# Kernel optimization log

Measured on AMD Instinct MI355X. Metric: run time of the kernel, lower is better.

The kernel has to match this reference:

```python
import jax, jax.numpy as jnp
import numpy as np

N_NODES = 100000
N_EDGES = 1600000
IN_CH = 48
OUT_CH = 48
BN_EPS = 1e-5


def setup_inputs() -> dict:
    key = jax.random.key(0)
    k1, k2, k3, k4 = jax.random.split(key, 4)
    x = jax.random.normal(k1, (N_NODES, IN_CH), dtype=jnp.float32)
    edge_index = jax.random.randint(k2, (2, N_EDGES), 0, N_NODES, dtype=jnp.int32)
    # GCNConv linear weight (glorot) and bias
    W = jax.random.normal(k3, (IN_CH, OUT_CH), dtype=jnp.float32) * (1.0 / np.sqrt(IN_CH))
    b = jnp.zeros((OUT_CH,), dtype=jnp.float32)
    # BatchNorm affine params
    gamma = jnp.ones((OUT_CH,), dtype=jnp.float32)
    beta = jnp.zeros((OUT_CH,), dtype=jnp.float32)
    return {"x": x, "edge_index": edge_index, "W": W, "b": b, "gamma": gamma, "beta": beta}


def reference(x, edge_index, W, b, gamma, beta):
    N = x.shape[0]
    # --- GCNConv: add self loops ---
    loops = jnp.arange(N, dtype=edge_index.dtype)
    src = jnp.concatenate([edge_index[0], loops])
    dst = jnp.concatenate([edge_index[1], loops])
    # symmetric normalization: deg counted at destination (incl. self loops)
    deg = jax.ops.segment_sum(jnp.ones_like(dst, dtype=x.dtype), dst, num_segments=N)
    dinv = jax.lax.rsqrt(deg)  # deg >= 1 due to self loops
    norm = dinv[src] * dinv[dst]  # [E+N]
    # linear transform first (small GEMM), then gather-scale-scatter
    h = x @ W  # [N, OUT_CH]
    msg = h[src] * norm[:, None]  # [E+N, OUT_CH]
    agg = jax.ops.segment_sum(msg, dst, num_segments=N) + b  # [N, OUT_CH]
    # --- BatchNorm1d (training mode: batch statistics, biased variance) ---
    mean = jnp.mean(agg, axis=0)
    var = jnp.mean(jnp.square(agg - mean), axis=0)
    y = (agg - mean) * jax.lax.rsqrt(var + BN_EPS) * gamma + beta
    # --- ReLU ---
    return jax.nn.relu(y)
```

## Files before the change

kernel.cpp:

```cpp
#include <hip/hip_runtime.h>
#include <hip/hip_bf16.h>

#define IN_CH 48
#define OUT_CH 48
#define BN_EPS 1e-5f
#define CHUNK 4096
#define EPT   16
#define NPB   256

__device__ __forceinline__ float bf2f(ushort u) {
    union { unsigned int i; float f; } v;
    v.i = ((unsigned int)u) << 16;
    return v.f;
}
__device__ __forceinline__ ushort f2bf(float f) {
    __hip_bfloat16 h = __float2bfloat16(f);
    return *(ushort*)&h;
}

__global__ __launch_bounds__(256) void k_binhist(const int* __restrict__ dst,
                                                 int* __restrict__ bhist, int E) {
    __shared__ int h[512];
    int t = threadIdx.x;
    h[t] = 0; h[t + 256] = 0;
    __syncthreads();
    for (int e = blockIdx.x * 256 + t; e < E; e += gridDim.x * 256)
        atomicAdd(&h[dst[e] >> 8], 1);
    __syncthreads();
    if (h[t]) atomicAdd(&bhist[t], h[t]);
    if (h[t + 256]) atomicAdd(&bhist[t + 256], h[t + 256]);
}

__global__ __launch_bounds__(256) void k_scanb(const int* __restrict__ bhist,
                                               int* __restrict__ bstart,
                                               int* __restrict__ bcur, int nb) {
    __shared__ int sc[256];
    int t = threadIdx.x;
    int i0 = 2 * t, i1 = 2 * t + 1;
    int a0 = bhist[i0];
    int a1 = bhist[i1];
    int ps = a0 + a1;
    sc[t] = ps;
    __syncthreads();
    for (int off = 1; off < 256; off <<= 1) {
        int v = (t >= off) ? sc[t - off] : 0;
        __syncthreads();
        sc[t] += v;
        __syncthreads();
    }
    int excl = sc[t] - ps;
    bstart[i0] = excl;
    bstart[i1] = excl + a0;
    if (i0 < nb) bcur[i0] = excl;
    if (i1 < nb) bcur[i1] = excl + a0;
    if (t == 255) bstart[512] = sc[255];
}

__global__ __launch_bounds__(256) void k_bin(const int* __restrict__ src,
                                             const int* __restrict__ dst,
                                             int* __restrict__ bcur,
                                             unsigned int* __restrict__ binned,
                                             int E) {
    __shared__ int hist[512];
    __shared__ int hbase[513];
    __shared__ int sc[256];
    __shared__ int gb[512];
    __shared__ unsigned int stage[CHUNK];
    __shared__ short stagebk[CHUNK];
    int t = threadIdx.x;
    int e0 = blockIdx.x * CHUNK;
    int n = min(CHUNK, E - e0);

    hist[t] = 0; hist[t + 256] = 0;
    __syncthreads();

    unsigned int w[EPT];
    short bb[EPT];
#pragma unroll
    for (int k = 0; k < EPT; ++k) {
        int i = t + k * 256;
        if (i < n) {
            int e = e0 + i;
            int s = src[e], d = dst[e];
            int b = d >> 8;
            w[k] = (unsigned int)s | ((unsigned int)(d & 255) << 17);
            bb[k] = (short)b;
            atomicAdd(&hist[b], 1);
        } else bb[k] = -1;
    }
    __syncthreads();
    int a0 = hist[2 * t], a1 = hist[2 * t + 1];
    int ps = a0 + a1;
    sc[t] = ps;
    __syncthreads();
    for (int off = 1; off < 256; off <<= 1) {
        int v = (t >= off) ? sc[t - off] : 0;
        __syncthreads();
        sc[t] += v;
        __syncthreads();
    }
    int excl = sc[t] - ps;
    hbase[2 * t] = excl;
    hbase[2 * t + 1] = excl + a0;
    if (t == 255) hbase[512] = sc[255];
    __syncthreads();
    hist[2 * t] = excl;
    hist[2 * t + 1] = excl + a0;
    __syncthreads();
#pragma unroll
    for (int k = 0; k < EPT; ++k) {
        if (bb[k] >= 0) {
            int pos = atomicAdd(&hist[bb[k]], 1);
            stage[pos] = w[k];
            stagebk[pos] = bb[k];
        }
    }
    __syncthreads();
    for (int b = t; b < 512; b += 256) {
        int cnt = hbase[b + 1] - hbase[b];
        if (cnt > 0) gb[b] = atomicAdd(&bcur[b], cnt) - hbase[b];
    }
    __syncthreads();
    for (int j = t; j < n; j += 256) {
        int bk = stagebk[j];
        binned[gb[bk] + j] = stage[j];
    }
}

__global__ __launch_bounds__(512) void k_fine(const unsigned int* __restrict__ binned,
                                              const int* __restrict__ bstart,
                                              int* __restrict__ counts,
                                              int* __restrict__ rowstart,
                                              int* __restrict__ sorted_src, int N) {
    __shared__ int cnt[256];
    __shared__ int sc[256];
    __shared__ int cur[256];
    int b = blockIdx.x, t = threadIdx.x;
    int node0 = b << 8;
    int nn = min(NPB, N - node0);
    if (t < 256) cnt[t] = 0;
    __syncthreads();
    int e0 = bstart[b], e1 = bstart[b + 1];
    for (int e = e0 + t; e < e1; e += 512)
        atomicAdd(&cnt[binned[e] >> 17], 1);
    __syncthreads();
    if (t < 256) sc[t] = cnt[t];
    __syncthreads();
    for (int off = 1; off < 256; off <<= 1) {
        int v = 0;
        if (t < 256 && t >= off) v = sc[t - off];
        __syncthreads();
        if (t < 256) sc[t] += v;
        __syncthreads();
    }
    if (t < 256) {
        int excl = sc[t] - cnt[t];
        cur[t] = e0 + excl;
        if (t < nn) {
            counts[node0 + t] = cnt[t];
            rowstart[node0 + t] = e0 + excl;
        }
    }
    __syncthreads();
    for (int e = e0 + t; e < e1; e += 512) {
        unsigned int w = binned[e];
        int dl = (int)(w >> 17);
        int pos = atomicAdd(&cur[dl], 1);
        sorted_src[pos] = (int)(w & 0x1ffff);
    }
}

__global__ __launch_bounds__(256) void k_gemm(const float* __restrict__ x,
                                              const float* __restrict__ W,
                                              const int* __restrict__ counts,
                                              ushort* __restrict__ g, int N) {
    __shared__ float Wl[IN_CH * OUT_CH];
    for (int idx = threadIdx.x; idx < IN_CH * OUT_CH / 4; idx += blockDim.x)
        ((float4*)Wl)[idx] = ((const float4*)W)[idx];
    __syncthreads();

    int i = blockIdx.x * blockDim.x + threadIdx.x;
    if (i >= N) return;

    float xr[IN_CH];
    const float4* xp = (const float4*)(x + (size_t)i * IN_CH);
#pragma unroll
    for (int k = 0; k < IN_CH / 4; ++k) {
        float4 v = xp[k];
        xr[4 * k] = v.x; xr[4 * k + 1] = v.y; xr[4 * k + 2] = v.z; xr[4 * k + 3] = v.w;
    }
    float di = rsqrtf((float)counts[i] + 1.0f);

    ushort row[OUT_CH];
#pragma unroll
    for (int c4 = 0; c4 < OUT_CH / 4; ++c4) {
        float4 acc = make_float4(0.f, 0.f, 0.f, 0.f);
#pragma unroll
        for (int k = 0; k < IN_CH; ++k) {
            float4 w = ((const float4*)Wl)[k * (OUT_CH / 4) + c4];
            acc.x += xr[k] * w.x; acc.y += xr[k] * w.y;
            acc.z += xr[k] * w.z; acc.w += xr[k] * w.w;
        }
        row[4 * c4 + 0] = f2bf(acc.x * di);
        row[4 * c4 + 1] = f2bf(acc.y * di);
        row[4 * c4 + 2] = f2bf(acc.z * di);
        row[4 * c4 + 3] = f2bf(acc.w * di);
    }
    uint4* gp = (uint4*)(g + (size_t)i * OUT_CH);
#pragma unroll
    for (int j = 0; j < 6; ++j) gp[j] = ((uint4*)row)[j];
}

__global__ __launch_bounds__(256) void k_gather(const int* __restrict__ sorted_src,
                                                const int* __restrict__ rowstart,
                                                const int* __restrict__ counts,
                                                const ushort* __restrict__ g,
                                                float* __restrict__ out, int N) {
    int t = blockIdx.x * blockDim.x + threadIdx.x;
    if (t >= N * 12) return;
    int node = t / 12;
    int sub = t - node * 12;
    const uint2* gp = (const uint2*)g;
    int cnt = counts[node];
    int e = rowstart[node];
    int end = e + cnt;

    uint2 sv = gp[(size_t)node * 12 + sub];
    float a0 = bf2f((ushort)(sv.x & 0xffff));
    float a1 = bf2f((ushort)(sv.x >> 16));
    float a2 = bf2f((ushort)(sv.y & 0xffff));
    float a3 = bf2f((ushort)(sv.y >> 16));

    for (; e + 4 <= end; e += 4) {
        int s0 = sorted_src[e];
        int s1 = sorted_src[e + 1];
        int s2 = sorted_src[e + 2];
        int s3 = sorted_src[e + 3];
        uint2 v0 = gp[(size_t)s0 * 12 + sub];
        uint2 v1 = gp[(size_t)s1 * 12 + sub];
        uint2 v2 = gp[(size_t)s2 * 12 + sub];
        uint2 v3 = gp[(size_t)s3 * 12 + sub];
        a0 += bf2f((ushort)(v0.x & 0xffff)) + bf2f((ushort)(v1.x & 0xffff))
            + bf2f((ushort)(v2.x & 0xffff)) + bf2f((ushort)(v3.x & 0xffff));
        a1 += bf2f((ushort)(v0.x >> 16)) + bf2f((ushort)(v1.x >> 16))
            + bf2f((ushort)(v2.x >> 16)) + bf2f((ushort)(v3.x >> 16));
        a2 += bf2f((ushort)(v0.y & 0xffff)) + bf2f((ushort)(v1.y & 0xffff))
            + bf2f((ushort)(v2.y & 0xffff)) + bf2f((ushort)(v3.y & 0xffff));
        a3 += bf2f((ushort)(v0.y >> 16)) + bf2f((ushort)(v1.y >> 16))
            + bf2f((ushort)(v2.y >> 16)) + bf2f((ushort)(v3.y >> 16));
    }
    for (; e < end; ++e) {
        int s = sorted_src[e];
        uint2 v = gp[(size_t)s * 12 + sub];
        a0 += bf2f((ushort)(v.x & 0xffff));
        a1 += bf2f((ushort)(v.x >> 16));
        a2 += bf2f((ushort)(v.y & 0xffff));
        a3 += bf2f((ushort)(v.y >> 16));
    }
    float di = rsqrtf((float)cnt + 1.0f);
    float4 r;
    r.x = a0 * di; r.y = a1 * di; r.z = a2 * di; r.w = a3 * di;
    ((float4*)out)[(size_t)node * 12 + sub] = r;
}

__global__ __launch_bounds__(768) void k_stats(const float* __restrict__ v,
                                               float* __restrict__ stats, int N) {
    __shared__ float ls[16][OUT_CH];
    __shared__ float ls2[16][OUT_CH];
    int c = threadIdx.x;
    int ty = threadIdx.y;
    float s = 0.f, s2 = 0.f;
    for (int r = blockIdx.x * 16 + ty; r < N; r += gridDim.x * 16) {
        float u = v[(size_t)r * OUT_CH + c];
        s += u;
        s2 += u * u;
    }
    ls[ty][c] = s;
    ls2[ty][c] = s2;
    __syncthreads();
    for (int h = 8; h > 0; h >>= 1) {
        if (ty < h) {
            ls[ty][c] += ls[ty + h][c];
            ls2[ty][c] += ls2[ty + h][c];
        }
        __syncthreads();
    }
    if (ty == 0) {
        atomicAdd(&stats[c], ls[0][c]);
        atomicAdd(&stats[OUT_CH + c], ls2[0][c]);
    }
}

__global__ void k_final(float* __restrict__ out, const float* __restrict__ stats,
                        const float* __restrict__ gamma,
                        const float* __restrict__ beta, int N) {
    int t = blockIdx.x * blockDim.x + threadIdx.x;
    int total = N * OUT_CH;
    if (t >= total) return;
    int c = t % OUT_CH;
    float invN = 1.0f / (float)N;
    float m = stats[c] * invN;
    float var = stats[OUT_CH + c] * invN - m * m;
    float y = (out[t] - m) * rsqrtf(var + BN_EPS) * gamma[c] + beta[c];
    out[t] = fmaxf(y, 0.0f);
}

extern "C" void kernel_launch(void* const* d_in, const int* in_sizes, int n_in,
                              void* d_out, int out_size, void* d_ws, size_t ws_size,
                              hipStream_t stream) {
    const float* x     = (const float*)d_in[0];
    const int*   ei    = (const int*)d_in[1];
    const float* W     = (const float*)d_in[2];
    const float* gamma = (const float*)d_in[4];
    const float* beta  = (const float*)d_in[5];
    float*       out   = (float*)d_out;

    int N = in_sizes[0] / IN_CH;
    int E = in_sizes[1] / 2;
    const int* src = ei;
    const int* dst = ei + E;

    int nb = (N + NPB - 1) / NPB;

    char* wsb = (char*)d_ws;
    int*          bhist      = (int*)wsb;
    float*        stats      = (float*)(wsb + 2048);
    int*          bstart     = (int*)(wsb + 2560);
    int*          bcur       = (int*)(wsb + 4640);
    int*          counts     = (int*)(wsb + 8192);
    int*          rowstart   = (int*)(wsb + 8192 + (size_t)4 * N);
    unsigned int* binned     = (unsigned int*)(wsb + 8192 + (size_t)8 * N);
    int*          sorted_src = (int*)(wsb + 8192 + (size_t)8 * N + (size_t)4 * E);
    ushort*       g          = (ushort*)(wsb + 8192 + (size_t)8 * N + (size_t)8 * E);

    int b = 256;

    hipMemsetAsync(d_ws, 0, 2560, stream);
    k_binhist<<<512, b, 0, stream>>>(dst, bhist, E);
    k_scanb<<<1, b, 0, stream>>>(bhist, bstart, bcur, nb);
    int nchunks = (E + CHUNK - 1) / CHUNK;
    k_bin<<<nchunks, b, 0, stream>>>(src, dst, bcur, binned, E);
    k_fine<<<nb, 512, 0, stream>>>(binned, bstart, counts, rowstart, sorted_src, N);
    k_gemm<<<(N + b - 1) / b, b, 0, stream>>>(x, W, counts, g, N);
    int gthreads = N * 12;
    k_gather<<<(gthreads + b - 1) / b, b, 0, stream>>>(sorted_src, rowstart, counts, g, out, N);
    dim3 sblk(OUT_CH, 16);
    k_stats<<<256, sblk, 0, stream>>>(out, stats, N);
    int totalT = N * OUT_CH;
    k_final<<<(totalT + b - 1) / b, b, 0, stream>>>(out, stats, gamma, beta, N);
}
```

Baseline: 140.7 us.

## Count degrees with global atomics early and fuse GEMM into binning kernel

Per-node in-degree counts are now computed in the histogram pass with global atomics, so the fine-sort kernel reads them instead of building its own shared-memory histogram. Because the degrees are ready earlier, the dense transform runs as extra blocks inside the coarse binning kernel, with shared memory held in a union. This removes one launch and lets the compute-bound GEMM overlap the memory-bound scatter. In exchange it adds 1.6M global atomics on counts, replaces the memset with a zeroing kernel, and gives GEMM blocks the larger shared-memory footprint of the binning path, which may lower their occupancy.

```diff
diff --git a/kernel.cpp b/kernel.cpp
--- a/kernel.cpp
+++ b/kernel.cpp
@@ -18,14 +18,31 @@
     return *(ushort*)&h;
 }
 
-__global__ __launch_bounds__(256) void k_binhist(const int* __restrict__ dst,
-                                                 int* __restrict__ bhist, int E) {
+__global__ __launch_bounds__(256) void k_zero(int* __restrict__ counts,
+                                              int* __restrict__ bhist,
+                                              float* __restrict__ stats, int N) {
+    int t = threadIdx.x;
+    int i = blockIdx.x * 256 + t;
+    if (i < N) counts[i] = 0;
+    if (blockIdx.x == 0) {
+        bhist[t] = 0;
+        bhist[t + 256] = 0;
+        if (t < 128) stats[t] = 0.0f;
+    }
+}
+
+__global__ __launch_bounds__(256) void k_cnt(const int* __restrict__ dst,
+                                             int* __restrict__ counts,
+                                             int* __restrict__ bhist, int E) {
     __shared__ int h[512];
     int t = threadIdx.x;
     h[t] = 0; h[t + 256] = 0;
     __syncthreads();
-    for (int e = blockIdx.x * 256 + t; e < E; e += gridDim.x * 256)
-        atomicAdd(&h[dst[e] >> 8], 1);
+    for (int e = blockIdx.x * 256 + t; e < E; e += gridDim.x * 256) {
+        int d = dst[e];
+        atomicAdd(&counts[d], 1);
+        atomicAdd(&h[d >> 8], 1);
+    }
     __syncthreads();
     if (h[t]) atomicAdd(&bhist[t], h[t]);
     if (h[t + 256]) atomicAdd(&bhist[t + 256], h[t + 256]);
@@ -56,95 +73,142 @@
     if (t == 255) bstart[512] = sc[255];
 }
 
-__global__ __launch_bounds__(256) void k_bin(const int* __restrict__ src,
-                                             const int* __restrict__ dst,
-                                             int* __restrict__ bcur,
-                                             unsigned int* __restrict__ binned,
-                                             int E) {
-    __shared__ int hist[512];
-    __shared__ int hbase[513];
-    __shared__ int sc[256];
-    __shared__ int gb[512];
-    __shared__ unsigned int stage[CHUNK];
-    __shared__ short stagebk[CHUNK];
+union alignas(16) SMem {
+    struct {
+        int hist[512];
+        int hbase[513];
+        int sc[256];
+        int gb[512];
+        unsigned int stage[CHUNK];
+        short stagebk[CHUNK];
+    } bin;
+    float Wl[IN_CH * OUT_CH];
+};
+
+__global__ __launch_bounds__(256) void k_binmm(const int* __restrict__ src,
+                                               const int* __restrict__ dst,
+                                               int* __restrict__ bcur,
+                                               unsigned int* __restrict__ binned,
+                                               int E, int nchunks,
+                                               const float* __restrict__ x,
+                                               const float* __restrict__ W,
+                                               const int* __restrict__ counts,
+                                               ushort* __restrict__ g, int N) {
+    __shared__ SMem sm;
     int t = threadIdx.x;
-    int e0 = blockIdx.x * CHUNK;
-    int n = min(CHUNK, E - e0);
-
-    hist[t] = 0; hist[t + 256] = 0;
-    __syncthreads();
-
-    unsigned int w[EPT];
-    short bb[EPT];
-#pragma unroll
-    for (int k = 0; k < EPT; ++k) {
-        int i = t + k * 256;
-        if (i < n) {
-            int e = e0 + i;
-            int s = src[e], d = dst[e];
-            int b = d >> 8;
-            w[k] = (unsigned int)s | ((unsigned int)(d & 255) << 17);
-            bb[k] = (short)b;
-            atomicAdd(&hist[b], 1);
-        } else bb[k] = -1;
-    }
-    __syncthreads();
-    int a0 = hist[2 * t], a1 = hist[2 * t + 1];
-    int ps = a0 + a1;
-    sc[t] = ps;
-    __syncthreads();
-    for (int off = 1; off < 256; off <<= 1) {
-        int v = (t >= off) ? sc[t - off] : 0;
-        __syncthreads();
-        sc[t] += v;
-        __syncthreads();
-    }
-    int excl = sc[t] - ps;
-    hbase[2 * t] = excl;
-    hbase[2 * t + 1] = excl + a0;
-    if (t == 255) hbase[512] = sc[255];
-    __syncthreads();
-    hist[2 * t] = excl;
-    hist[2 * t + 1] = excl + a0;
-    __syncthreads();
-#pragma unroll
-    for (int k = 0; k < EPT; ++k) {
-        if (bb[k] >= 0) {
-            int pos = atomicAdd(&hist[bb[k]], 1);
-            stage[pos] = w[k];
-            stagebk[pos] = bb[k];
-        }
-    }
-    __syncthreads();
-    for (int b = t; b < 512; b += 256) {
-        int cnt = hbase[b + 1] - hbase[b];
-        if (cnt > 0) gb[b] = atomicAdd(&bcur[b], cnt) - hbase[b];
-    }
-    __syncthreads();
-    for (int j = t; j < n; j += 256) {
-        int bk = stagebk[j];
-        binned[gb[bk] + j] = stage[j];
+
+    if (blockIdx.x < nchunks) {
+        int e0 = blockIdx.x * CHUNK;
+        int n = min(CHUNK, E - e0);
+
+        sm.bin.hist[t] = 0; sm.bin.hist[t + 256] = 0;
+        __syncthreads();
+
+        unsigned int w[EPT];
+        short bb[EPT];
+#pragma unroll
+        for (int k = 0; k < EPT; ++k) {
+            int i = t + k * 256;
+            if (i < n) {
+                int e = e0 + i;
+                int s = src[e], d = dst[e];
+                int b = d >> 8;
+                w[k] = (unsigned int)s | ((unsigned int)(d & 255) << 17);
+                bb[k] = (short)b;
+                atomicAdd(&sm.bin.hist[b], 1);
+            } else bb[k] = -1;
+        }
+        __syncthreads();
+        int a0 = sm.bin.hist[2 * t], a1 = sm.bin.hist[2 * t + 1];
+        int ps = a0 + a1;
+        sm.bin.sc[t] = ps;
+        __syncthreads();
+        for (int off = 1; off < 256; off <<= 1) {
+            int v = (t >= off) ? sm.bin.sc[t - off] : 0;
+            __syncthreads();
+            sm.bin.sc[t] += v;
+            __syncthreads();
+        }
+        int excl = sm.bin.sc[t] - ps;
+        sm.bin.hbase[2 * t] = excl;
+        sm.bin.hbase[2 * t + 1] = excl + a0;
+        if (t == 255) sm.bin.hbase[512] = sm.bin.sc[255];
+        __syncthreads();
+        sm.bin.hist[2 * t] = excl;
+        sm.bin.hist[2 * t + 1] = excl + a0;
+        __syncthreads();
+#pragma unroll
+        for (int k = 0; k < EPT; ++k) {
+            if (bb[k] >= 0) {
+                int pos = atomicAdd(&sm.bin.hist[bb[k]], 1);
+                sm.bin.stage[pos] = w[k];
+                sm.bin.stagebk[pos] = bb[k];
+            }
+        }
+        __syncthreads();
+        for (int b = t; b < 512; b += 256) {
+            int cnt = sm.bin.hbase[b + 1] - sm.bin.hbase[b];
+            if (cnt > 0) sm.bin.gb[b] = atomicAdd(&bcur[b], cnt) - sm.bin.hbase[b];
+        }
+        __syncthreads();
+        for (int j = t; j < n; j += 256) {
+            int bk = sm.bin.stagebk[j];
+            binned[sm.bin.gb[bk] + j] = sm.bin.stage[j];
+        }
+    } else {
+        for (int idx = t; idx < IN_CH * OUT_CH / 4; idx += 256)
+            ((float4*)sm.Wl)[idx] = ((const float4*)W)[idx];
+        __syncthreads();
+
+        int i = (blockIdx.x - nchunks) * 256 + t;
+        if (i >= N) return;
+
+        float xr[IN_CH];
+        const float4* xp = (const float4*)(x + (size_t)i * IN_CH);
+#pragma unroll
+        for (int k = 0; k < IN_CH / 4; ++k) {
+            float4 v = xp[k];
+            xr[4 * k] = v.x; xr[4 * k + 1] = v.y; xr[4 * k + 2] = v.z; xr[4 * k + 3] = v.w;
+        }
+        float di = rsqrtf((float)counts[i] + 1.0f);
+
+        ushort row[OUT_CH];
+#pragma unroll
+        for (int c4 = 0; c4 < OUT_CH / 4; ++c4) {
+            float4 acc = make_float4(0.f, 0.f, 0.f, 0.f);
+#pragma unroll
+            for (int k = 0; k < IN_CH; ++k) {
+                float4 wv = ((const float4*)sm.Wl)[k * (OUT_CH / 4) + c4];
+                acc.x += xr[k] * wv.x; acc.y += xr[k] * wv.y;
+                acc.z += xr[k] * wv.z; acc.w += xr[k] * wv.w;
+            }
+            row[4 * c4 + 0] = f2bf(acc.x * di);
+            row[4 * c4 + 1] = f2bf(acc.y * di);
+            row[4 * c4 + 2] = f2bf(acc.z * di);
+            row[4 * c4 + 3] = f2bf(acc.w * di);
+        }
+        uint4* gp = (uint4*)(g + (size_t)i * OUT_CH);
+#pragma unroll
+        for (int j = 0; j < 6; ++j) gp[j] = ((uint4*)row)[j];
     }
 }
 
 __global__ __launch_bounds__(512) void k_fine(const unsigned int* __restrict__ binned,
                                               const int* __restrict__ bstart,
-                                              int* __restrict__ counts,
+                                              const int* __restrict__ counts,
                                               int* __restrict__ rowstart,
                                               int* __restrict__ sorted_src, int N) {
-    __shared__ int cnt[256];
     __shared__ int sc[256];
     __shared__ int cur[256];
     int b = blockIdx.x, t = threadIdx.x;
     int node0 = b << 8;
     int nn = min(NPB, N - node0);
-    if (t < 256) cnt[t] = 0;
-    __syncthreads();
     int e0 = bstart[b], e1 = bstart[b + 1];
-    for (int e = e0 + t; e < e1; e += 512)
-        atomicAdd(&cnt[binned[e] >> 17], 1);
-    __syncthreads();
-    if (t < 256) sc[t] = cnt[t];
+    int c = 0;
+    if (t < 256) {
+        c = (t < nn) ? counts[node0 + t] : 0;
+        sc[t] = c;
+    }
     __syncthreads();
     for (int off = 1; off < 256; off <<= 1) {
         int v = 0;
@@ -154,12 +218,9 @@
         __syncthreads();
     }
     if (t < 256) {
-        int excl = sc[t] - cnt[t];
+        int excl = sc[t] - c;
         cur[t] = e0 + excl;
-        if (t < nn) {
-            counts[node0 + t] = cnt[t];
-            rowstart[node0 + t] = e0 + excl;
-        }
+        if (t < nn) rowstart[node0 + t] = e0 + excl;
     }
     __syncthreads();
     for (int e = e0 + t; e < e1; e += 512) {
@@ -168,47 +229,6 @@
         int pos = atomicAdd(&cur[dl], 1);
         sorted_src[pos] = (int)(w & 0x1ffff);
     }
-}
-
-__global__ __launch_bounds__(256) void k_gemm(const float* __restrict__ x,
-                                              const float* __restrict__ W,
-                                              const int* __restrict__ counts,
-                                              ushort* __restrict__ g, int N) {
-    __shared__ float Wl[IN_CH * OUT_CH];
-    for (int idx = threadIdx.x; idx < IN_CH * OUT_CH / 4; idx += blockDim.x)
-        ((float4*)Wl)[idx] = ((const float4*)W)[idx];
-    __syncthreads();
-
-    int i = blockIdx.x * blockDim.x + threadIdx.x;
-    if (i >= N) return;
-
-    float xr[IN_CH];
-    const float4* xp = (const float4*)(x + (size_t)i * IN_CH);
-#pragma unroll
-    for (int k = 0; k < IN_CH / 4; ++k) {
-        float4 v = xp[k];
-        xr[4 * k] = v.x; xr[4 * k + 1] = v.y; xr[4 * k + 2] = v.z; xr[4 * k + 3] = v.w;
-    }
-    float di = rsqrtf((float)counts[i] + 1.0f);
-
-    ushort row[OUT_CH];
-#pragma unroll
-    for (int c4 = 0; c4 < OUT_CH / 4; ++c4) {
-        float4 acc = make_float4(0.f, 0.f, 0.f, 0.f);
-#pragma unroll
-        for (int k = 0; k < IN_CH; ++k) {
-            float4 w = ((const float4*)Wl)[k * (OUT_CH / 4) + c4];
-            acc.x += xr[k] * w.x; acc.y += xr[k] * w.y;
-            acc.z += xr[k] * w.z; acc.w += xr[k] * w.w;
-        }
-        row[4 * c4 + 0] = f2bf(acc.x * di);
-        row[4 * c4 + 1] = f2bf(acc.y * di);
-        row[4 * c4 + 2] = f2bf(acc.z * di);
-        row[4 * c4 + 3] = f2bf(acc.w * di);
-    }
-    uint4* gp = (uint4*)(g + (size_t)i * OUT_CH);
-#pragma unroll
-    for (int j = 0; j < 6; ++j) gp[j] = ((uint4*)row)[j];
 }
 
 __global__ __launch_bounds__(256) void k_gather(const int* __restrict__ sorted_src,
@@ -334,14 +354,16 @@
     ushort*       g          = (ushort*)(wsb + 8192 + (size_t)8 * N + (size_t)8 * E);
 
     int b = 256;
-
-    hipMemsetAsync(d_ws, 0, 2560, stream);
-    k_binhist<<<512, b, 0, stream>>>(dst, bhist, E);
+    int nzero = (N + b - 1) / b;
+    int nchunks = (E + CHUNK - 1) / CHUNK;
+    int ngemm = (N + b - 1) / b;
+
+    k_zero<<<nzero, b, 0, stream>>>(counts, bhist, stats, N);
+    k_cnt<<<512, b, 0, stream>>>(dst, counts, bhist, E);
     k_scanb<<<1, b, 0, stream>>>(bhist, bstart, bcur, nb);
-    int nchunks = (E + CHUNK - 1) / CHUNK;
-    k_bin<<<nchunks, b, 0, stream>>>(src, dst, bcur, binned, E);
+    k_binmm<<<nchunks + ngemm, b, 0, stream>>>(src, dst, bcur, binned, E, nchunks,
+                                               x, W, counts, g, N);
     k_fine<<<nb, 512, 0, stream>>>(binned, bstart, counts, rowstart, sorted_src, N);
-    k_gemm<<<(N + b - 1) / b, b, 0, stream>>>(x, W, counts, g, N);
     int gthreads = N * 12;
     k_gather<<<(gthreads + b - 1) / b, b, 0, stream>>>(sorted_src, rowstart, counts, g, out, N);
     dim3 sblk(OUT_CH, 16);
```

After: 189.8 us. 1.35x slower.
